# Kernel optimization log

Measured on AMD Instinct MI355X. Metric: run time of the kernel, lower is better.

## Reference

```python
import jax, jax.numpy as jnp
import numpy as np

# ---- config (matches init_kwargs) ----
ORIGIN_OCC_SHAPE = (16, 200, 200)   # (D_oi, H_oi, W_oi)
INPUT_SIZE = (900, 1600)            # (ih, iw)
DOWN_SAMPLE = 8
GRID_CONFIG = {
    'x_bound': [-40.0, 40.0, 0.4],
    'y_bound': [-40.0, 40.0, 0.4],
    'z_bound': [-1.0, 5.4, 0.4],
    'd_bound': [2.0, 58.0, 1.0],
}


def setup_inputs() -> dict:
    key = jax.random.key(0)
    occ_feature = jax.random.normal(key, (1, 32, 16, 200, 200), dtype=jnp.float32)
    # realistic nuScenes-like intrinsics
    K = jnp.array([[[1266.4, 0.0, 816.3],
                    [0.0, 1266.4, 491.5],
                    [0.0, 0.0, 1.0]]], dtype=jnp.float32)
    # cam->ego: camera looks along ego +x; cam z -> ego x, cam x -> ego -y, cam y -> ego -z
    T = jnp.array([[[0.0, 0.0, 1.0, 1.5],
                    [-1.0, 0.0, 0.0, 0.0],
                    [0.0, -1.0, 0.0, 1.5],
                    [0.0, 0.0, 0.0, 1.0]]], dtype=jnp.float32)
    return {'occ_feature': occ_feature, 'K': K, 'T': T}


def get_sampling_points():
    ih, iw = INPUT_SIZE
    fh, fw = ih // DOWN_SAMPLE, iw // DOWN_SAMPLE
    d0, d1, dstep = GRID_CONFIG['d_bound']
    fd = int((d1 - d0) // dstep)
    x = jnp.linspace(0.0, iw - 1.0, fw)
    y = jnp.linspace(0.0, ih - 1.0, fh)
    d = jnp.linspace(d0, d1, fd)
    gd, gy, gx = jnp.meshgrid(d, y, x, indexing='ij')   # (fd, fh, fw)
    # homogeneous image points scaled by depth: [x*d, y*d, d, 1]
    pts = jnp.stack([gx * gd, gy * gd, gd, jnp.ones_like(gd)], axis=-1)
    return pts  # (fd, fh, fw, 4)


def grid_sample_3d(vol, grid):
    """Trilinear grid_sample, padding_mode='zeros', align_corners=True.
    vol: (B,C,D,H,W); grid: (B,Do,Ho,Wo,3) with (x,y,z) in [-1,1] -> (W,H,D)."""
    B, C, D, H, W = vol.shape
    gx, gy, gz = grid[..., 0], grid[..., 1], grid[..., 2]
    x = (gx + 1.0) * 0.5 * (W - 1)
    y = (gy + 1.0) * 0.5 * (H - 1)
    z = (gz + 1.0) * 0.5 * (D - 1)
    x0 = jnp.floor(x); y0 = jnp.floor(y); z0 = jnp.floor(z)
    tx = x - x0; ty = y - y0; tz = z - z0
    vol_flat = vol.reshape(B, C, D * H * W)

    def corner(zc, yc, xc, w):
        valid = (xc >= 0) & (xc <= W - 1) & (yc >= 0) & (yc <= H - 1) & (zc >= 0) & (zc <= D - 1)
        zi = jnp.clip(zc, 0, D - 1).astype(jnp.int32)
        yi = jnp.clip(yc, 0, H - 1).astype(jnp.int32)
        xi = jnp.clip(xc, 0, W - 1).astype(jnp.int32)
        idx = ((zi * H + yi) * W + xi).reshape(B, 1, -1)          # (B,1,M)
        g = jnp.take_along_axis(vol_flat, idx, axis=2)            # (B,C,M)
        wm = jnp.where(valid, w, 0.0).reshape(B, 1, -1)
        return g * wm

    out = (corner(z0, y0, x0, (1 - tz) * (1 - ty) * (1 - tx))
           + corner(z0, y0, x0 + 1, (1 - tz) * (1 - ty) * tx)
           + corner(z0, y0 + 1, x0, (1 - tz) * ty * (1 - tx))
           + corner(z0, y0 + 1, x0 + 1, (1 - tz) * ty * tx)
           + corner(z0 + 1, y0, x0, tz * (1 - ty) * (1 - tx))
           + corner(z0 + 1, y0, x0 + 1, tz * (1 - ty) * tx)
           + corner(z0 + 1, y0 + 1, x0, tz * ty * (1 - tx))
           + corner(z0 + 1, y0 + 1, x0 + 1, tz * ty * tx))
    Do, Ho, Wo = grid.shape[1:4]
    return out.reshape(B, C, Do, Ho, Wo)


def volume_transform(occ_feature, K, T):
    B, C, D_occ, H_occ, W_occ = occ_feature.shape
    D_oi, H_oi, W_oi = ORIGIN_OCC_SHAPE
    ratio = (W_oi / W_occ, H_oi / H_occ, D_oi / D_occ)
    xb, yb, zb = GRID_CONFIG['x_bound'], GRID_CONFIG['y_bound'], GRID_CONFIG['z_bound']

    # ego -> ego-feature-grid affine (4x4)
    e2f = jnp.eye(4, dtype=jnp.float32)
    e2f = e2f.at[0, 0].set(1.0 / xb[2] / ratio[0])
    e2f = e2f.at[1, 1].set(1.0 / yb[2] / ratio[1])
    e2f = e2f.at[2, 2].set(1.0 / zb[2] / ratio[2])
    e2f = e2f.at[0, 3].set(-xb[0] / xb[2] / ratio[0])
    e2f = e2f.at[1, 3].set(-yb[0] / yb[2] / ratio[1])
    e2f = e2f.at[2, 3].set(-zb[0] / zb[2] / ratio[2])

    # cam2img 4x4 with K in top-left, then invert (matches torch.inverse path)
    cam2img = jnp.tile(jnp.eye(4, dtype=K.dtype)[None], (B, 1, 1))
    cam2img = cam2img.at[:, :3, :3].set(K)
    img2cam = jnp.linalg.inv(cam2img)                  # (B,4,4)

    # fused projection matrix: ego2egofeat @ T @ img2cam
    M = jnp.einsum('ij,bjk,bkl->bil', e2f, T, img2cam)  # (B,4,4)

    pts = get_sampling_points()                         # (fd,fh,fw,4)
    feat_pts = jnp.einsum('bij,dhwj->bdhwi', M, pts)[..., :3]  # (B,fd,fh,fw,3)

    norm = jnp.array([W_occ - 1, H_occ - 1, D_occ - 1], dtype=jnp.float32)
    grid = feat_pts / norm * 2.0 - 1.0

    sampled = grid_sample_3d(occ_feature, grid)         # (B,C,fd,fh,fw)
    return jnp.sum(sampled, axis=2)                     # (B,C,fh,fw)


def reference(occ_feature, K, T):
    return volume_transform(occ_feature, K, T)
```

## Files before the change

kernel.cpp:

```cpp
#include <hip/hip_runtime.h>

#define FD 56
#define FH 112
#define FW 200
#define VD 16
#define VH 200
#define VW 200
#define NC 32
#define NPIX (FH * FW)
#define NS   (VD * VH * VW)
#define CSTRIDE NS

typedef float f2v __attribute__((ext_vector_type(2)));
typedef f2v uf2v4 __attribute__((aligned(4)));
typedef _Float16 h4 __attribute__((ext_vector_type(4)));
typedef h4 uh4 __attribute__((aligned(8)));
typedef _Float16 h8 __attribute__((ext_vector_type(8)));

__device__ inline void compute_M(const float* Km, const float* Tm, float* M) {
    float a = Km[0], b = Km[1], c = Km[2];
    float d = Km[3], e = Km[4], f = Km[5];
    float g = Km[6], h = Km[7], i = Km[8];
    float A00 = e * i - f * h, A01 = c * h - b * i, A02 = b * f - c * e;
    float A10 = f * g - d * i, A11 = a * i - c * g, A12 = c * d - a * f;
    float A20 = d * h - e * g, A21 = b * g - a * h, A22 = a * e - b * d;
    float det = a * A00 + b * A10 + c * A20;
    float r = 1.0f / det;
    float Ki[9] = {A00 * r, A01 * r, A02 * r,
                   A10 * r, A11 * r, A12 * r,
                   A20 * r, A21 * r, A22 * r};
    float R[4][4];
    for (int rr = 0; rr < 4; ++rr) {
        for (int cc = 0; cc < 3; ++cc)
            R[rr][cc] = Tm[rr * 4 + 0] * Ki[0 * 3 + cc]
                      + Tm[rr * 4 + 1] * Ki[1 * 3 + cc]
                      + Tm[rr * 4 + 2] * Ki[2 * 3 + cc];
        R[rr][3] = Tm[rr * 4 + 3];
    }
    const float s[3] = {2.5f, 2.5f, 2.5f};
    const float t[3] = {100.0f, 100.0f, 2.5f};
    for (int rr = 0; rr < 3; ++rr)
        for (int cc = 0; cc < 4; ++cc)
            M[rr * 4 + cc] = s[rr] * R[rr][cc] + t[rr] * R[3][cc];
}

__device__ inline void compute_crop(const float* m, int& cx0, int& cy0, int& cz0,
                                    int& cw, int& ch, int& cd) {
    const int l = threadIdx.x & 63;
    int bx0 = 0x7fffffff, by0 = 0x7fffffff, bz0 = 0x7fffffff;
    int bx1 = -1, by1 = -1, bz1 = -1;
    if (l < FD) {
        const float gd = 2.0f + (float)l * (56.0f / 55.0f);
        const float HIq[3] = {(float)VW, (float)VH, (float)VD};
        float lo[3], hi[3];
        bool ok = true;
#pragma unroll
        for (int q = 0; q < 3; ++q) {
            const float axx  = m[q * 4 + 0] * gd * 1599.0f;
            const float byy  = m[q * 4 + 1] * gd * 899.0f;
            const float base = m[q * 4 + 2] * gd + m[q * 4 + 3];
            lo[q] = base + fminf(axx, 0.0f) + fminf(byy, 0.0f);
            hi[q] = base + fmaxf(axx, 0.0f) + fmaxf(byy, 0.0f);
            if (!(lo[q] < HIq[q] && hi[q] > -1.0f)) ok = false;
        }
        if (ok) {
            const int dmax[3] = {VW - 1, VH - 1, VD - 1};
#pragma unroll
            for (int q = 0; q < 3; ++q) {
                int i0 = (int)floorf(fmaxf(lo[q], -2.0f)) - 1;
                int i1 = (int)floorf(fminf(hi[q], HIq[q] + 1.0f)) + 2;
                i0 = max(i0, 0);
                i1 = min(i1, dmax[q]);
                if (q == 0) { bx0 = i0; bx1 = i1; }
                else if (q == 1) { by0 = i0; by1 = i1; }
                else { bz0 = i0; bz1 = i1; }
            }
        }
    }
#pragma unroll
    for (int s = 1; s < 64; s <<= 1) {
        bx0 = min(bx0, __shfl_xor(bx0, s));
        bx1 = max(bx1, __shfl_xor(bx1, s));
        by0 = min(by0, __shfl_xor(by0, s));
        by1 = max(by1, __shfl_xor(by1, s));
        bz0 = min(bz0, __shfl_xor(bz0, s));
        bz1 = max(bz1, __shfl_xor(bz1, s));
    }
    if (bx1 < bx0 || by1 < by0 || bz1 < bz0) {
        bx0 = by0 = bz0 = 0; bx1 = by1 = bz1 = 0;
    }
    cx0 = bx0; cy0 = by0; cz0 = bz0;
    cw = bx1 - bx0 + 1; ch = by1 - by0 + 1; cd = bz1 - bz0 + 1;
}

__device__ inline int wedge_skip(const float* M, const float lo[3], const float hi[3]) {
    const float b00 = M[0], b01 = M[1], b02 = M[2],  tx3 = M[3];
    const float b10 = M[4], b11 = M[5], b12 = M[6],  ty3 = M[7];
    const float b20 = M[8], b21 = M[9], b22 = M[10], tz3 = M[11];
    const float C00 = b11 * b22 - b12 * b21;
    const float C01 = b02 * b21 - b01 * b22;
    const float C02 = b01 * b12 - b02 * b11;
    const float C10 = b12 * b20 - b10 * b22;
    const float C11 = b00 * b22 - b02 * b20;
    const float C12 = b02 * b10 - b00 * b12;
    const float C20 = b10 * b21 - b11 * b20;
    const float C21 = b01 * b20 - b00 * b21;
    const float C22 = b00 * b11 - b01 * b10;
    const float det = b00 * C00 + b01 * C10 + b02 * C20;
    if (!(fabsf(det) > 1e-12f)) return 0;
    const float r = 1.0f / det;
    const float ix0 = C00 * r, ix1 = C01 * r, ix2 = C02 * r;
    const float iy0 = C10 * r, iy1 = C11 * r, iy2 = C12 * r;
    const float iz0 = C20 * r, iz1 = C21 * r, iz2 = C22 * r;
    const float cx = -(ix0 * tx3 + ix1 * ty3 + ix2 * tz3);
    const float cy = -(iy0 * tx3 + iy1 * ty3 + iy2 * tz3);
    const float cz = -(iz0 * tx3 + iz1 * ty3 + iz2 * tz3);
    const float SLK = 10.0f;
    const float gc[6][3] = {
        { iz0,  iz1,  iz2},
        {-iz0, -iz1, -iz2},
        { ix0,  ix1,  ix2},
        {1599.f*iz0 - ix0, 1599.f*iz1 - ix1, 1599.f*iz2 - ix2},
        { iy0,  iy1,  iy2},
        { 899.f*iz0 - iy0,  899.f*iz1 - iy1,  899.f*iz2 - iy2},
    };
    const float gd0[6] = {cz - 2.0f + 0.1f, 58.0f + 0.1f - cz,
                          cx + SLK, 1599.f * cz - cx + SLK,
                          cy + SLK,  899.f * cz - cy + SLK};
    for (int q = 0; q < 6; ++q) {
        float mx = gd0[q];
        for (int j = 0; j < 3; ++j)
            mx += (gc[q][j] > 0.0f) ? gc[q][j] * hi[j] : gc[q][j] * lo[j];
        if (mx < 0.0f) return 1;
    }
    return 0;
}

__global__ __launch_bounds__(256)
void vt_transpose_c(const float* __restrict__ vol, _Float16* __restrict__ volT,
                    const float* __restrict__ Km, const float* __restrict__ Tm) {
    __shared__ float tile[256 * 33];
    const int t = threadIdx.x;

    float M[12];
    compute_M(Km, Tm, M);
    int x0, y0, z0, cw, ch, cd;
    compute_crop(M, x0, y0, z0, cw, ch, cd);
    const int chw = ch * cw;
    const int tot = cd * chw;
    const int cb0 = blockIdx.x * 256;
    if (cb0 >= tot) return;

    {
        const int clast = min(cb0 + 255, tot - 1);
        const int ez0 = cb0 / chw, ez1 = clast / chw;
        int ey0 = 0, ey1 = ch - 1;
        if (ez0 == ez1) {
            const int r0 = cb0 - ez0 * chw;
            ey0 = r0 / cw;
            ey1 = (clast - ez0 * chw) / cw;
        }
        const float EXP = 1.25f;
        const float lo[3] = {(float)x0 - EXP, (float)(y0 + ey0) - EXP, (float)(z0 + ez0) - EXP};
        const float hi[3] = {(float)(x0 + cw - 1) + EXP, (float)(y0 + ey1) + EXP, (float)(z0 + ez1) + EXP};
        if (wedge_skip(M, lo, hi)) return;
    }

    const int cidx = cb0 + t;
    const bool live = cidx < tot;
    int lin = 0;
    if (live) {
        const int ez = cidx / chw;
        const int r1 = cidx - ez * chw;
        const int ey = r1 / cw;
        const int ex = r1 - ey * cw;
        lin = (z0 + ez) * (VH * VW) + (y0 + ey) * VW + (x0 + ex);
    }
    if (live) {
#pragma unroll
        for (int c = 0; c < NC; ++c)
            tile[t * 33 + c] = __builtin_nontemporal_load(vol + (size_t)c * CSTRIDE + lin);
    }
    __syncthreads();
    const int rs  = t >> 2;
    const int ch8 = (t & 3) * 8;
#pragma unroll
    for (int j = 0; j < 4; ++j) {
        const int sl = j * 64 + rs;
        if (cb0 + sl >= tot) continue;
        const float* r = &tile[sl * 33 + ch8];
        h8 pk = {(_Float16)r[0], (_Float16)r[1], (_Float16)r[2], (_Float16)r[3],
                 (_Float16)r[4], (_Float16)r[5], (_Float16)r[6], (_Float16)r[7]};
        *(h8*)(volT + ((size_t)(cb0 + sl) << 5) + ch8) = pk;
    }
}

__global__ __launch_bounds__(256)
void vt_sample_c(const _Float16* __restrict__ volT,
                 const float* __restrict__ Km,
                 const float* __restrict__ Tm,
                 float* __restrict__ out) {
    float Mv[12];
    compute_M(Km, Tm, Mv);
    int x0, y0, z0, cw, chh, cd;
    compute_crop(Mv, x0, y0, z0, cw, chh, cd);
    const int X0 = x0, X1 = x0 + cw - 1;
    const int Y0 = y0, Y1 = y0 + chh - 1;
    const int Z0 = z0, Z1 = z0 + cd - 1;
    const int CWr = cw, CHWr = chh * cw;

    const int t    = threadIdx.x;
    const int wv   = t >> 6;
    const int lane = t & 63;
    const int chq  = lane & 7;
    const int pixl = lane >> 3;
    const int c0   = chq * 4;
    const int p    = blockIdx.x * 32 + wv * 8 + pixl;
    const int py   = p / FW;
    const int px   = p - py * FW;

    const float gx = (float)px * (1599.0f / 199.0f);
    const float gy = (float)py * (899.0f / 111.0f);

    const float m03 = Mv[3], m13 = Mv[7], m23 = Mv[11];
    const float ax = Mv[0] * gx + Mv[1] * gy + Mv[2];
    const float ay = Mv[4] * gx + Mv[5] * gy + Mv[6];
    const float az = Mv[8] * gx + Mv[9] * gy + Mv[10];

    float dlo = 2.0f, dhi = 58.0f;
    {
        const float A[3]  = {ax, ay, az};
        const float Bv[3] = {m03, m13, m23};
        const float HI[3] = {(float)VW, (float)VH, (float)VD};
        for (int q = 0; q < 3; ++q) {
            float a = A[q], b = Bv[q], hi = HI[q];
            if (a > 0.0f)      { dlo = fmaxf(dlo, (-1.0f - b) / a); dhi = fminf(dhi, (hi - b) / a); }
            else if (a < 0.0f) { dlo = fmaxf(dlo, (hi - b) / a);    dhi = fminf(dhi, (-1.0f - b) / a); }
            else if (!(b > -1.0f && b < hi)) { dlo = 1e30f; dhi = -1e30f; }
        }
    }
    int klo = (int)ceilf((dlo - 2.0f) * (55.0f / 56.0f));
    int khi = (int)floorf((dhi - 2.0f) * (55.0f / 56.0f));
    klo = max(klo - 1, 0);
    khi = min(khi + 1, FD - 1);

    float acc0 = 0.0f, acc1 = 0.0f, acc2 = 0.0f, acc3 = 0.0f;

#pragma unroll 2
    for (int k = klo; k <= khi; ++k) {
        const float gd = 2.0f + (float)k * (56.0f / 55.0f);
        const float fx = fmaf(ax, gd, m03);
        const float fy = fmaf(ay, gd, m13);
        const float fz = fmaf(az, gd, m23);

        const bool valid = (fx > -1.0f) && (fx < (float)VW) &&
                           (fy > -1.0f) && (fy < (float)VH) &&
                           (fz > -1.0f) && (fz < (float)VD);
        const float vm = valid ? 1.0f : 0.0f;

        const float xf = floorf(fx), yf = floorf(fy), zf = floorf(fz);
        const float tx = fx - xf, ty = fy - yf, tz = fz - zf;
        const int ix = (int)xf, iy = (int)yf, iz = (int)zf;

        const float wx0 = (ix >= 0)     ? (1.0f - tx) : 0.0f;
        const float wx1 = (ix < VW - 1) ? tx          : 0.0f;
        const float wy0 = (iy >= 0)     ? (1.0f - ty) : 0.0f;
        const float wy1 = (iy < VH - 1) ? ty          : 0.0f;
        const float wz0 = ((iz >= 0)     ? (1.0f - tz) : 0.0f) * vm;
        const float wz1 = ((iz < VD - 1) ? tz          : 0.0f) * vm;

        const int xi0 = min(max(ix,     X0), X1) - X0;
        const int xi1 = min(max(ix + 1, X0), X1) - X0;
        const int yo0 = (min(max(iy,     Y0), Y1) - Y0) * CWr;
        const int yo1 = (min(max(iy + 1, Y0), Y1) - Y0) * CWr;
        const int zo0 = (min(max(iz,     Z0), Z1) - Z0) * CHWr;
        const int zo1 = (min(max(iz + 1, Z0), Z1) - Z0) * CHWr;

        const int o000 = ((zo0 + yo0 + xi0) << 5) + c0;
        const int o001 = ((zo0 + yo0 + xi1) << 5) + c0;
        const int o010 = ((zo0 + yo1 + xi0) << 5) + c0;
        const int o011 = ((zo0 + yo1 + xi1) << 5) + c0;
        const int o100 = ((zo1 + yo0 + xi0) << 5) + c0;
        const int o101 = ((zo1 + yo0 + xi1) << 5) + c0;
        const int o110 = ((zo1 + yo1 + xi0) << 5) + c0;
        const int o111 = ((zo1 + yo1 + xi1) << 5) + c0;

        const h4 v000 = *(const uh4*)(volT + o000);
        const h4 v001 = *(const uh4*)(volT + o001);
        const h4 v010 = *(const uh4*)(volT + o010);
        const h4 v011 = *(const uh4*)(volT + o011);
        const h4 v100 = *(const uh4*)(volT + o100);
        const h4 v101 = *(const uh4*)(volT + o101);
        const h4 v110 = *(const uh4*)(volT + o110);
        const h4 v111 = *(const uh4*)(volT + o111);

        const float w000 = wz0 * wy0 * wx0, w001 = wz0 * wy0 * wx1;
        const float w010 = wz0 * wy1 * wx0, w011 = wz0 * wy1 * wx1;
        const float w100 = wz1 * wy0 * wx0, w101 = wz1 * wy0 * wx1;
        const float w110 = wz1 * wy1 * wx0, w111 = wz1 * wy1 * wx1;

        acc0 += w000 * (float)v000.x + w001 * (float)v001.x
              + w010 * (float)v010.x + w011 * (float)v011.x
              + w100 * (float)v100.x + w101 * (float)v101.x
              + w110 * (float)v110.x + w111 * (float)v111.x;
        acc1 += w000 * (float)v000.y + w001 * (float)v001.y
              + w010 * (float)v010.y + w011 * (float)v011.y
              + w100 * (float)v100.y + w101 * (float)v101.y
              + w110 * (float)v110.y + w111 * (float)v111.y;
        acc2 += w000 * (float)v000.z + w001 * (float)v001.z
              + w010 * (float)v010.z + w011 * (float)v011.z
              + w100 * (float)v100.z + w101 * (float)v101.z
              + w110 * (float)v110.z + w111 * (float)v111.z;
        acc3 += w000 * (float)v000.w + w001 * (float)v001.w
              + w010 * (float)v010.w + w011 * (float)v011.w
              + w100 * (float)v100.w + w101 * (float)v101.w
              + w110 * (float)v110.w + w111 * (float)v111.w;
    }

    out[(size_t)(c0 + 0) * NPIX + p] = acc0;
    out[(size_t)(c0 + 1) * NPIX + p] = acc1;
    out[(size_t)(c0 + 2) * NPIX + p] = acc2;
    out[(size_t)(c0 + 3) * NPIX + p] = acc3;
}

__global__ __launch_bounds__(256)
void vt_sample_direct(const float* __restrict__ vol,
                      const float* __restrict__ Km,
                      const float* __restrict__ Tm,
                      float* __restrict__ out) {
    __shared__ float sM[12];
    if (threadIdx.x == 0) compute_M(Km, Tm, sM);
    __syncthreads();

    const int cg   = blockIdx.x & 3;
    const int pg   = blockIdx.x >> 2;
    const int lane = threadIdx.x & 63;
    const int wv   = threadIdx.x >> 6;
    const int c0   = (cg * 4 + wv) * 2;
    const int p    = pg * 64 + lane;
    const int py   = p / FW;
    const int px   = p - py * FW;

    const float gx = (float)px * (1599.0f / 199.0f);
    const float gy = (float)py * (899.0f / 111.0f);

    const float m03 = sM[3], m13 = sM[7], m23 = sM[11];
    const float ax = sM[0] * gx + sM[1] * gy + sM[2];
    const float ay = sM[4] * gx + sM[5] * gy + sM[6];
    const float az = sM[8] * gx + sM[9] * gy + sM[10];

    float dlo = 2.0f, dhi = 58.0f;
    {
        const float A[3]  = {ax, ay, az};
        const float Bv[3] = {m03, m13, m23};
        const float HI[3] = {(float)VW, (float)VH, (float)VD};
        for (int q = 0; q < 3; ++q) {
            float a = A[q], b = Bv[q], hi = HI[q];
            if (a > 0.0f)      { dlo = fmaxf(dlo, (-1.0f - b) / a); dhi = fminf(dhi, (hi - b) / a); }
            else if (a < 0.0f) { dlo = fmaxf(dlo, (hi - b) / a);    dhi = fminf(dhi, (-1.0f - b) / a); }
            else if (!(b > -1.0f && b < hi)) { dlo = 1e30f; dhi = -1e30f; }
        }
    }
    int klo = (int)ceilf((dlo - 2.0f) * (55.0f / 56.0f));
    int khi = (int)floorf((dhi - 2.0f) * (55.0f / 56.0f));
    klo = max(klo - 1, 0);
    khi = min(khi + 1, FD - 1);

    const float* __restrict__ volc0 = vol + (size_t)c0 * CSTRIDE;
    const float* __restrict__ volc1 = volc0 + CSTRIDE;
    float acc0 = 0.0f, acc1 = 0.0f;

#pragma unroll 2
    for (int k = klo; k <= khi; ++k) {
        const float gd = 2.0f + (float)k * (56.0f / 55.0f);
        const float fx = fmaf(ax, gd, m03);
        const float fy = fmaf(ay, gd, m13);
        const float fz = fmaf(az, gd, m23);

        const bool valid = (fx > -1.0f) && (fx < (float)VW) &&
                           (fy > -1.0f) && (fy < (float)VH) &&
                           (fz > -1.0f) && (fz < (float)VD);
        const float vm = valid ? 1.0f : 0.0f;

        const float xf = floorf(fx), yf = floorf(fy), zf = floorf(fz);
        const float tx = fx - xf, ty = fy - yf, tz = fz - zf;
        const int ix = (int)xf, iy = (int)yf, iz = (int)zf;

        float wlo = (ix >= 0) ? (1.0f - tx) : tx;
        wlo = (ix >= VW - 1) ? 0.0f : wlo;
        float whi = (ix >= 0) ? tx : 0.0f;
        whi = (ix >= VW - 1) ? (1.0f - tx) : whi;

        const float wy0 = (iy >= 0)     ? (1.0f - ty) : 0.0f;
        const float wy1 = (iy < VH - 1) ? ty          : 0.0f;
        const float wz0 = ((iz >= 0)     ? (1.0f - tz) : 0.0f) * vm;
        const float wz1 = ((iz < VD - 1) ? tz          : 0.0f) * vm;
        const float w00 = wz0 * wy0, w01 = wz0 * wy1;
        const float w10 = wz1 * wy0, w11 = wz1 * wy1;

        const int xi0 = min(max(ix, 0), VW - 2);
        const int yo0 = min(max(iy,     0), VH - 1) * VW;
        const int yo1 = min(max(iy + 1, 0), VH - 1) * VW;
        const int zo0 = min(max(iz,     0), VD - 1) * (VH * VW);
        const int zo1 = min(max(iz + 1, 0), VD - 1) * (VH * VW);

        const int o00 = zo0 + yo0 + xi0, o01 = zo0 + yo1 + xi0;
        const int o10 = zo1 + yo0 + xi0, o11 = zo1 + yo1 + xi0;

        const f2v a00 = *(const uf2v4*)(volc0 + o00);
        const f2v a01 = *(const uf2v4*)(volc0 + o01);
        const f2v a10 = *(const uf2v4*)(volc0 + o10);
        const f2v a11 = *(const uf2v4*)(volc0 + o11);
        const f2v b00 = *(const uf2v4*)(volc1 + o00);
        const f2v b01 = *(const uf2v4*)(volc1 + o01);
        const f2v b10 = *(const uf2v4*)(volc1 + o10);
        const f2v b11 = *(const uf2v4*)(volc1 + o11);

        acc0 += w00 * (wlo * a00.x + whi * a00.y) + w01 * (wlo * a01.x + whi * a01.y)
              + w10 * (wlo * a10.x + whi * a10.y) + w11 * (wlo * a11.x + whi * a11.y);
        acc1 += w00 * (wlo * b00.x + whi * b00.y) + w01 * (wlo * b01.x + whi * b01.y)
              + w10 * (wlo * b10.x + whi * b10.y) + w11 * (wlo * b11.x + whi * b11.y);
    }

    out[c0 * NPIX + p]       = acc0;
    out[(c0 + 1) * NPIX + p] = acc1;
}

extern "C" void kernel_launch(void* const* d_in, const int* in_sizes, int n_in,
                              void* d_out, int out_size, void* d_ws, size_t ws_size,
                              hipStream_t stream) {
    (void)in_sizes; (void)n_in; (void)out_size;
    const float* vol = (const float*)d_in[0];
    const float* Km  = (const float*)d_in[1];
    const float* Tm  = (const float*)d_in[2];
    float* out = (float*)d_out;

    const size_t need = (size_t)NS * NC * sizeof(_Float16);
    if (ws_size >= need) {
        _Float16* volT = (_Float16*)d_ws;
        vt_transpose_c<<<dim3(NS / 256), dim3(256), 0, stream>>>(vol, volT, Km, Tm);
        vt_sample_c<<<dim3(NPIX / 32), dim3(256), 0, stream>>>(volT, Km, Tm, out);
    } else {
        vt_sample_direct<<<dim3(1400), dim3(256), 0, stream>>>(vol, Km, Tm, out);
    }
}
```

Measured before the change: 144.0 us.

## Split depth loop across waves and widen per-lane channel loads to 8

The sampling kernel now assigns 8 channels per lane (16-byte fp16 loads) and 16 pixels per block. The four waves of a block split the depth samples in a strided fashion and combine their partial sums through shared memory before writing. This aims to balance per-pixel depth-range work and issue fewer, wider gather loads, at the cost of a block-wide barrier and a shared-memory reduction.

```diff
diff --git a/kernel.cpp b/kernel.cpp
--- a/kernel.cpp
+++ b/kernel.cpp
@@ -13,9 +13,9 @@
 
 typedef float f2v __attribute__((ext_vector_type(2)));
 typedef f2v uf2v4 __attribute__((aligned(4)));
-typedef _Float16 h4 __attribute__((ext_vector_type(4)));
-typedef h4 uh4 __attribute__((aligned(8)));
+typedef float f8v __attribute__((ext_vector_type(8)));
 typedef _Float16 h8 __attribute__((ext_vector_type(8)));
+typedef h8 uh8 __attribute__((aligned(16)));
 
 __device__ inline void compute_M(const float* Km, const float* Tm, float* M) {
     float a = Km[0], b = Km[1], c = Km[2];
@@ -200,6 +200,7 @@
                  const float* __restrict__ Km,
                  const float* __restrict__ Tm,
                  float* __restrict__ out) {
+    __shared__ f8v red[3][64];
     float Mv[12];
     compute_M(Km, Tm, Mv);
     int x0, y0, z0, cw, chh, cd;
@@ -210,12 +211,12 @@
     const int CWr = cw, CHWr = chh * cw;
 
     const int t    = threadIdx.x;
-    const int wv   = t >> 6;
+    const int kh   = t >> 6;
     const int lane = t & 63;
-    const int chq  = lane & 7;
-    const int pixl = lane >> 3;
-    const int c0   = chq * 4;
-    const int p    = blockIdx.x * 32 + wv * 8 + pixl;
+    const int chq  = lane & 3;
+    const int pixl = lane >> 2;
+    const int c0   = chq * 8;
+    const int p    = blockIdx.x * 16 + pixl;
     const int py   = p / FW;
     const int px   = p - py * FW;
 
@@ -244,10 +245,10 @@
     klo = max(klo - 1, 0);
     khi = min(khi + 1, FD - 1);
 
-    float acc0 = 0.0f, acc1 = 0.0f, acc2 = 0.0f, acc3 = 0.0f;
+    f8v acc = {0.0f, 0.0f, 0.0f, 0.0f, 0.0f, 0.0f, 0.0f, 0.0f};
 
 #pragma unroll 2
-    for (int k = klo; k <= khi; ++k) {
+    for (int k = klo + kh; k <= khi; k += 4) {
         const float gd = 2.0f + (float)k * (56.0f / 55.0f);
         const float fx = fmaf(ax, gd, m03);
         const float fy = fmaf(ay, gd, m13);
@@ -285,42 +286,40 @@
         const int o110 = ((zo1 + yo1 + xi0) << 5) + c0;
         const int o111 = ((zo1 + yo1 + xi1) << 5) + c0;
 
-        const h4 v000 = *(const uh4*)(volT + o000);
-        const h4 v001 = *(const uh4*)(volT + o001);
-        const h4 v010 = *(const uh4*)(volT + o010);
-        const h4 v011 = *(const uh4*)(volT + o011);
-        const h4 v100 = *(const uh4*)(volT + o100);
-        const h4 v101 = *(const uh4*)(volT + o101);
-        const h4 v110 = *(const uh4*)(volT + o110);
-        const h4 v111 = *(const uh4*)(volT + o111);
+        const h8 v000 = *(const uh8*)(volT + o000);
+        const h8 v001 = *(const uh8*)(volT + o001);
+        const h8 v010 = *(const uh8*)(volT + o010);
+        const h8 v011 = *(const uh8*)(volT + o011);
+        const h8 v100 = *(const uh8*)(volT + o100);
+        const h8 v101 = *(const uh8*)(volT + o101);
+        const h8 v110 = *(const uh8*)(volT + o110);
+        const h8 v111 = *(const uh8*)(volT + o111);
 
         const float w000 = wz0 * wy0 * wx0, w001 = wz0 * wy0 * wx1;
         const float w010 = wz0 * wy1 * wx0, w011 = wz0 * wy1 * wx1;
         const float w100 = wz1 * wy0 * wx0, w101 = wz1 * wy0 * wx1;
         const float w110 = wz1 * wy1 * wx0, w111 = wz1 * wy1 * wx1;
 
-        acc0 += w000 * (float)v000.x + w001 * (float)v001.x
-              + w010 * (float)v010.x + w011 * (float)v011.x
-              + w100 * (float)v100.x + w101 * (float)v101.x
-              + w110 * (float)v110.x + w111 * (float)v111.x;
-        acc1 += w000 * (float)v000.y + w001 * (float)v001.y
-              + w010 * (float)v010.y + w011 * (float)v011.y
-              + w100 * (float)v100.y + w101 * (float)v101.y
-              + w110 * (float)v110.y + w111 * (float)v111.y;
-        acc2 += w000 * (float)v000.z + w001 * (float)v001.z
-              + w010 * (float)v010.z + w011 * (float)v011.z
-              + w100 * (float)v100.z + w101 * (float)v101.z
-              + w110 * (float)v110.z + w111 * (float)v111.z;
-        acc3 += w000 * (float)v000.w + w001 * (float)v001.w
-              + w010 * (float)v010.w + w011 * (float)v011.w
-              + w100 * (float)v100.w + w101 * (float)v101.w
-              + w110 * (float)v110.w + w111 * (float)v111.w;
-    }
-
-    out[(size_t)(c0 + 0) * NPIX + p] = acc0;
-    out[(size_t)(c0 + 1) * NPIX + p] = acc1;
-    out[(size_t)(c0 + 2) * NPIX + p] = acc2;
-    out[(size_t)(c0 + 3) * NPIX + p] = acc3;
+#pragma unroll
+        for (int j = 0; j < 8; ++j) {
+            acc[j] += w000 * (float)v000[j] + w001 * (float)v001[j]
+                    + w010 * (float)v010[j] + w011 * (float)v011[j]
+                    + w100 * (float)v100[j] + w101 * (float)v101[j]
+                    + w110 * (float)v110[j] + w111 * (float)v111[j];
+        }
+    }
+
+    if (kh) red[kh - 1][lane] = acc;
+    __syncthreads();
+    if (kh == 0) {
+        const f8v r0 = red[0][lane];
+        const f8v r1 = red[1][lane];
+        const f8v r2 = red[2][lane];
+#pragma unroll
+        for (int j = 0; j < 8; ++j) {
+            out[(size_t)(c0 + j) * NPIX + p] = acc[j] + r0[j] + r1[j] + r2[j];
+        }
+    }
 }
 
 __global__ __launch_bounds__(256)
@@ -439,7 +438,7 @@
     if (ws_size >= need) {
         _Float16* volT = (_Float16*)d_ws;
         vt_transpose_c<<<dim3(NS / 256), dim3(256), 0, stream>>>(vol, volT, Km, Tm);
-        vt_sample_c<<<dim3(NPIX / 32), dim3(256), 0, stream>>>(volT, Km, Tm, out);
+        vt_sample_c<<<dim3(NPIX / 16), dim3(256), 0, stream>>>(volT, Km, Tm, out);
     } else {
         vt_sample_direct<<<dim3(1400), dim3(256), 0, stream>>>(vol, Km, Tm, out);
     }
```

Result: faster. 134.1 us (-6.8%).
